# Kernel tuning notes

Hardware: AMD Instinct MI355X
Metric: run time of the kernel (lower is better)

Reference implementation:

```python
import jax, jax.numpy as jnp
import numpy as np

EPS = 1e-12
NEG = -1e30
TOPK = 20

def l2norm(x, axis):
    n = jnp.sqrt(jnp.sum(x * x, axis=axis, keepdims=True))
    return x / jnp.maximum(n, EPS)

def setup_inputs() -> dict:
    key = jax.random.key(0)
    ks = jax.random.split(key, 12)
    B, R, W, D = 128, 36, 60, 1024
    img_regions = jax.random.normal(ks[0], (B, R, D), dtype=jnp.float32)
    cap_words = jax.random.normal(ks[1], (B, W, D), dtype=jnp.float32)
    cap_len = jax.random.randint(ks[2], (B,), 10, W + 1, dtype=jnp.int32)
    s = 0.1
    return {
        "img_regions": img_regions,
        "cap_words": cap_words,
        "w1_t2i": jax.random.normal(ks[3], (TOPK, TOPK), jnp.float32) * s,
        "b1_t2i": jnp.zeros((TOPK,), jnp.float32),
        "w2_t2i": jax.random.normal(ks[4], (TOPK,), jnp.float32) * s,
        "b2_t2i": jnp.zeros((), jnp.float32),
        "w1_i2t": jax.random.normal(ks[5], (TOPK, TOPK), jnp.float32) * s,
        "b1_i2t": jnp.zeros((TOPK,), jnp.float32),
        "w2_i2t": jax.random.normal(ks[6], (TOPK,), jnp.float32) * s,
        "b2_i2t": jnp.zeros((), jnp.float32),
        "cap_len": cap_len,
    }

def _mlp(x, w1, b1, w2, b2):
    h = jax.nn.relu(x @ w1 + b1)
    return h @ w2 + b2  # Linear(topk,1).squeeze(-1)

def reference(img_regions, cap_words, w1_t2i, b1_t2i, w2_t2i, b2_t2i,
              w1_i2t, b1_i2t, w2_i2t, b2_i2t, cap_len):
    C, W, D = cap_words.shape
    I, R, _ = img_regions.shape
    img_n = l2norm(img_regions, -1)            # [I,R,D]
    cap_n = l2norm(cap_words, -1)              # [C,W,D]
    # all caption x image pair similarities: sim[c,i,w,r]
    sim = jnp.einsum('cwd,ird->ciwr', cap_n, img_n)
    sim = jnp.where(sim >= 0, sim, 0.1 * sim)  # leaky_relu(0.1) (scan=True)
    num_sel = jnp.maximum(cap_len, TOPK)       # num_selected_word per caption
    w_idx = jnp.arange(W)
    sel_mask = (w_idx[None, :] < num_sel[:, None])  # [C,W]
    cap_mask = (w_idx[None, :] < cap_len[:, None])  # [C,W]
    sel4 = sel_mask[:, None, :, None]

    # ---- t2i (row) path: normalize over word axis among selected words ----
    sim_w = sim * sel4
    norm_w = jnp.sqrt(jnp.sum(sim_w * sim_w, axis=2, keepdims=True))
    sim_w = sim_w / jnp.maximum(norm_w, EPS)
    row_sim = jnp.max(sim_w, axis=3)                      # [C,I,W]
    row_sim = jnp.where(sel_mask[:, None, :], row_sim, NEG)
    row_mean = jnp.sum(jnp.where(cap_mask[:, None, :], row_sim, 0.0), axis=2) \
               / cap_len[:, None].astype(jnp.float32)     # [C,I]
    row_topk = jax.lax.top_k(row_sim, TOPK)[0]            # [C,I,K]

    # ---- i2t (column) path: normalize over region axis, max over real words ----
    norm_r = jnp.sqrt(jnp.sum(sim * sim, axis=3, keepdims=True))
    sim_r = sim / jnp.maximum(norm_r, EPS)
    col_sim = jnp.max(jnp.where(cap_mask[:, None, :, None], sim_r, NEG), axis=2)  # [C,I,R]
    col_mean = jnp.mean(col_sim, axis=2)                  # [C,I]
    col_topk = jax.lax.top_k(col_sim, TOPK)[0]            # [C,I,K]

    batch_t2i = row_topk                                   # [C,I,K]
    batch_t2i_mean = row_mean                              # [C,I]
    batch_i2t = jnp.transpose(col_topk, (1, 0, 2))         # [I,C,K]
    batch_i2t_mean = jnp.transpose(col_mean, (1, 0))       # [I,C]

    t2i_rel = _mlp(batch_t2i, w1_t2i, b1_t2i, w2_t2i, b2_t2i) + batch_t2i_mean
    i2t_rel = _mlp(batch_i2t, w1_i2t, b1_i2t, w2_i2t, b2_i2t) + batch_i2t_mean
    return (t2i_rel, i2t_rel, batch_t2i_mean, batch_i2t_mean)
```

## Files before the change

### kernel.cpp

```cpp
#include <hip/hip_runtime.h>
#include <hip/hip_bf16.h>
#include <cstdint>
#include <cstddef>

#define C_ 128
#define I_ 128
#define W_ 60
#define R_ 36
#define D_ 1024
#define TOPK 20
#define NEGV (-1e30f)
#define EPSV (1e-12f)

typedef __attribute__((ext_vector_type(8))) short bf16x8;
typedef __attribute__((ext_vector_type(4))) float f32x4;
typedef __attribute__((ext_vector_type(4))) int i32x4;

__device__ inline float bf2f(unsigned short u) {
    union { unsigned int i; float f; } x;
    x.i = ((unsigned int)u) << 16;
    return x.f;
}
__device__ inline unsigned short f2bf(float f) {
    __hip_bfloat16 h = __float2bfloat16(f);
    return *(unsigned short*)&h;
}
__device__ inline float wave_sum(float v) {
    #pragma unroll
    for (int o = 32; o; o >>= 1) v += __shfl_xor(v, o);
    return v;
}
__device__ inline float wave_max(float v) {
    #pragma unroll
    for (int o = 32; o; o >>= 1) v = fmaxf(v, __shfl_xor(v, o));
    return v;
}
__device__ inline float loadw(const void* p, int idx, bool isF32) {
    if (isF32) return ((const float*)p)[idx];
    return bf2f(((const unsigned short*)p)[idx]);
}
__device__ inline void dma16(const void* g, void* l) {
    __builtin_amdgcn_global_load_lds(
        (const __attribute__((address_space(1))) unsigned int*)g,
        (__attribute__((address_space(3))) unsigned int*)l, 16, 0, 0);
}

__device__ inline float bitonic64_desc(float v, int lane) {
    #pragma unroll
    for (int k = 2; k <= 64; k <<= 1) {
        #pragma unroll
        for (int j = k >> 1; j > 0; j >>= 1) {
            float o = __shfl_xor(v, j);
            bool keepMax = (((lane & k) == 0) == ((lane & j) == 0));
            v = keepMax ? fmaxf(v, o) : fminf(v, o);
        }
    }
    return v;
}

__device__ inline float topk_mlp2(float val, int lane,
                                  const float* __restrict__ w1g,
                                  const float* __restrict__ b1g,
                                  const float* __restrict__ w2g, float b2v) {
    float s = bitonic64_desc(val, lane);
    float h = 0.f;
    if (lane < TOPK) h = b1g[lane];
    #pragma unroll
    for (int k = 0; k < TOPK; ++k) {
        float sk = __shfl(s, k);
        if (lane < TOPK) h += sk * w1g[k * TOPK + lane];
    }
    float contrib = 0.f;
    if (lane < TOPK) contrib = fmaxf(h, 0.f) * w2g[lane];
    contrib = wave_sum(contrib);
    return contrib + b2v;
}

__global__ __launch_bounds__(256) void prep_norm3(
    const void* __restrict__ img, const void* __restrict__ cap,
    const void* __restrict__ w1_t2i, const void* __restrict__ b1_t2i,
    const void* __restrict__ w2_t2i, const void* __restrict__ b2_t2i,
    const void* __restrict__ w1_i2t, const void* __restrict__ b1_i2t,
    const void* __restrict__ w2_i2t, const void* __restrict__ b2_i2t,
    unsigned short* __restrict__ outN, float* __restrict__ wsW) {
    int t = threadIdx.x;
    int lane = t & 63;
    int wv = t >> 6;
    unsigned int probe = ((const unsigned int*)img)[lane];
    float pa = fmaxf(__builtin_fabsf(bf2f(probe & 0xffff)),
                     __builtin_fabsf(bf2f(probe >> 16)));
    bool isF32 = __ballot(pa > 1e6f) != 0ULL;

    int row = blockIdx.x * 4 + wv;
    const void* src; int srow;
    if (row < I_ * R_) { src = img; srow = row; }
    else               { src = cap; srow = row - I_ * R_; }

    float v[16];
    if (isF32) {
        const float* p = (const float*)src + (size_t)srow * D_;
        #pragma unroll
        for (int q = 0; q < 4; ++q) {
            float4 r = *(const float4*)(p + 4 * (lane + 64 * q));
            v[4 * q] = r.x; v[4 * q + 1] = r.y; v[4 * q + 2] = r.z; v[4 * q + 3] = r.w;
        }
    } else {
        const unsigned short* p = (const unsigned short*)src + (size_t)srow * D_;
        #pragma unroll
        for (int q = 0; q < 2; ++q) {
            uint4 r = *(const uint4*)(p + 8 * (lane + 64 * q));
            v[8 * q + 0] = bf2f(r.x & 0xffff); v[8 * q + 1] = bf2f(r.x >> 16);
            v[8 * q + 2] = bf2f(r.y & 0xffff); v[8 * q + 3] = bf2f(r.y >> 16);
            v[8 * q + 4] = bf2f(r.z & 0xffff); v[8 * q + 5] = bf2f(r.z >> 16);
            v[8 * q + 6] = bf2f(r.w & 0xffff); v[8 * q + 7] = bf2f(r.w >> 16);
        }
    }
    float ss = 0.f;
    #pragma unroll
    for (int q = 0; q < 16; ++q) ss += v[q] * v[q];
    ss = wave_sum(ss);
    float s = 1.0f / fmaxf(sqrtf(ss), EPSV);
    unsigned short* dst = outN + (size_t)row * D_;
    if (isF32) {
        #pragma unroll
        for (int q = 0; q < 4; ++q) {
            uint2 w;
            w.x = (unsigned)f2bf(v[4 * q] * s)     | ((unsigned)f2bf(v[4 * q + 1] * s) << 16);
            w.y = (unsigned)f2bf(v[4 * q + 2] * s) | ((unsigned)f2bf(v[4 * q + 3] * s) << 16);
            *(uint2*)(dst + 4 * (lane + 64 * q)) = w;
        }
    } else {
        #pragma unroll
        for (int q = 0; q < 2; ++q) {
            uint4 w;
            w.x = (unsigned)f2bf(v[8 * q + 0] * s) | ((unsigned)f2bf(v[8 * q + 1] * s) << 16);
            w.y = (unsigned)f2bf(v[8 * q + 2] * s) | ((unsigned)f2bf(v[8 * q + 3] * s) << 16);
            w.z = (unsigned)f2bf(v[8 * q + 4] * s) | ((unsigned)f2bf(v[8 * q + 5] * s) << 16);
            w.w = (unsigned)f2bf(v[8 * q + 6] * s) | ((unsigned)f2bf(v[8 * q + 7] * s) << 16);
            *(uint4*)(dst + 8 * (lane + 64 * q)) = w;
        }
    }
    if (blockIdx.x == 0) {
        for (int idx = t; idx < 400; idx += 256) {
            wsW[idx]       = loadw(w1_t2i, idx, isF32);
            wsW[400 + idx] = loadw(w1_i2t, idx, isF32);
        }
        if (t < 20) {
            wsW[800 + t] = loadw(b1_t2i, t, isF32);
            wsW[820 + t] = loadw(b1_i2t, t, isF32);
            wsW[840 + t] = loadw(w2_t2i, t, isF32);
            wsW[860 + t] = loadw(w2_i2t, t, isF32);
        }
        if (t == 0) { wsW[880] = loadw(b2_t2i, 0, isF32); wsW[881] = loadw(b2_i2t, 0, isF32); }
    }
}

#define SSB 148

struct __align__(16) Smem4 {
    union {
        struct { short A[128 * 64]; short B[144 * 64]; } st;
        unsigned short Sb[120 * SSB];
    } u;
    float nw[8][36];
    float nr[8][60];
};

__global__ __launch_bounds__(256, 4) void adj_main4(
    const unsigned short* __restrict__ capN, const unsigned short* __restrict__ imgN,
    const float* __restrict__ wsW, const int* __restrict__ cap_len,
    float* __restrict__ out) {
    __shared__ Smem4 sm;
    int tid = threadIdx.x;
    int lane = tid & 63;
    int wid = tid >> 6;
    int bx = blockIdx.x;
    int cg = bx & 63;
    int ig = bx >> 6;
    int c0 = cg * 2;
    int i0 = ig * 4;

    float b2a = wsW[880], b2b = wsW[881];

    f32x4 acc0[9], acc1[9];
    #pragma unroll
    for (int t = 0; t < 9; ++t) {
        acc0[t] = (f32x4){0.f, 0.f, 0.f, 0.f};
        acc1[t] = (f32x4){0.f, 0.f, 0.f, 0.f};
    }

    const unsigned short* capB = capN + (size_t)c0 * 60 * D_;
    const unsigned short* imgB = imgN + (size_t)i0 * 36 * D_;

    int quad = lane >> 4;
    int l16 = lane & 15;
    int sub = lane >> 3;
    int q8 = (lane & 7) ^ sub;

    for (int kc = 0; kc < 16; ++kc) {
        int kb = kc * 64;
        #pragma unroll
        for (int u = 0; u < 4; ++u) {
            int wo = (wid << 2) + u;
            int r = (wo << 3) + sub;
            int ar = r < 120 ? r : 119;
            dma16(capB + (size_t)ar * D_ + kb + q8 * 8,
                  (char*)sm.u.st.A + (wo << 10));
        }
        for (int wo = wid; wo < 18; wo += 4) {
            int r = (wo << 3) + sub;
            dma16(imgB + (size_t)r * D_ + kb + q8 * 8,
                  (char*)sm.u.st.B + (wo << 10));
        }
        __syncthreads();
        #pragma unroll
        for (int ks = 0; ks < 2; ++ks) {
            int swz = ((quad + 4 * ks) ^ (l16 & 7)) << 3;
            int rowA0 = (wid << 4) + l16;
            int rowA1 = ((wid + 4) << 4) + l16;
            bf16x8 a0 = *(const bf16x8*)(sm.u.st.A + rowA0 * 64 + swz);
            bf16x8 a1 = *(const bf16x8*)(sm.u.st.A + rowA1 * 64 + swz);
            #pragma unroll
            for (int t = 0; t < 9; ++t) {
                int rowB = (t << 4) + l16;
                bf16x8 b = *(const bf16x8*)(sm.u.st.B + rowB * 64 + swz);
                acc0[t] = __builtin_amdgcn_mfma_f32_16x16x32_bf16(a0, b, acc0[t], 0, 0, 0);
                acc1[t] = __builtin_amdgcn_mfma_f32_16x16x32_bf16(a1, b, acc1[t], 0, 0, 0);
            }
        }
        __syncthreads();
    }
    #pragma unroll
    for (int t = 0; t < 9; ++t) {
        int col = 16 * t + l16;
        #pragma unroll
        for (int v = 0; v < 4; ++v) {
            int row0 = wid * 16 + quad * 4 + v;
            float x0 = acc0[t][v];
            x0 = x0 >= 0.f ? x0 : 0.1f * x0;
            sm.u.Sb[row0 * SSB + col] = f2bf(x0);
            int row1 = 64 + wid * 16 + quad * 4 + v;
            if (row1 < 120) {
                float x1 = acc1[t][v];
                x1 = x1 >= 0.f ? x1 : 0.1f * x1;
                sm.u.Sb[row1 * SSB + col] = f2bf(x1);
            }
        }
    }
    __syncthreads();

    #pragma unroll 1
    for (int pp = 0; pp < 2; ++pp) {
        int p = wid + pp * 4;
        int cc = p >> 2, j = p & 3;
        int c = c0 + cc, i = i0 + j;
        int sbase = cc * 60;
        int cbase = j * 36;
        int L = cap_len[c];
        if (L < 1) L = 1;
        if (L > 60) L = 60;
        int Msel = L > TOPK ? L : TOPK;

        if (lane < 36) {
            float ssum = 0.f;
            for (int w = 0; w < Msel; ++w) {
                float v = bf2f(sm.u.Sb[(sbase + w) * SSB + cbase + lane]);
                ssum += v * v;
            }
            sm.nw[p][lane] = 1.0f / fmaxf(sqrtf(ssum), EPSV);
        }
        if (lane < 60) {
            float ssum = 0.f;
            for (int r = 0; r < 36; ++r) {
                float v = bf2f(sm.u.Sb[(sbase + lane) * SSB + cbase + r]);
                ssum += v * v;
            }
            sm.nr[p][lane] = 1.0f / fmaxf(sqrtf(ssum), EPSV);
        }

        float rs = NEGV;
        if (lane < Msel) {
            float m = -3.4e38f;
            for (int r = 0; r < 36; ++r) {
                float v = bf2f(sm.u.Sb[(sbase + lane) * SSB + cbase + r]);
                m = fmaxf(m, v * sm.nw[p][r]);
            }
            rs = m;
        }
        float msum = (lane < L) ? rs : 0.f;
        msum = wave_sum(msum);
        float row_mean = msum / (float)L;

        float t2i = topk_mlp2(rs, lane, wsW, wsW + 800, wsW + 840, b2a) + row_mean;
        if (lane == 0) {
            out[(size_t)c * 128 + i] = t2i;
            out[2 * 16384 + (size_t)c * 128 + i] = row_mean;
        }

        float cs = NEGV;
        if (lane < 36) {
            float m = -3.4e38f;
            for (int w = 0; w < L; ++w) {
                float v = bf2f(sm.u.Sb[(sbase + w) * SSB + cbase + lane]);
                m = fmaxf(m, v * sm.nr[p][w]);
            }
            cs = m;
        }
        float csum = (lane < 36) ? cs : 0.f;
        csum = wave_sum(csum);
        float col_mean = csum / 36.f;

        float i2t = topk_mlp2(cs, lane, wsW + 400, wsW + 820, wsW + 860, b2b) + col_mean;
        if (lane == 0) {
            out[16384 + (size_t)i * 128 + c] = i2t;
            out[3 * 16384 + (size_t)i * 128 + c] = col_mean;
        }
    }
}

__device__ inline float topk_mlp(float val, int lane,
                                 const float* __restrict__ w1,
                                 const float* __restrict__ b1,
                                 const float* __restrict__ w2, float b2v) {
    float tk[TOPK];
    #pragma unroll 1
    for (int k = 0; k < TOPK; ++k) {
        float m = wave_max(val);
        tk[k] = m;
        unsigned long long msk = __ballot(val == m);
        int first = __ffsll(msk) - 1;
        if (first >= 0 && lane == first) val = NEGV;
    }
    float contrib = 0.f;
    if (lane < TOPK) {
        float h = b1[lane];
        #pragma unroll 1
        for (int k = 0; k < TOPK; ++k)
            h += tk[k] * w1[k * TOPK + lane];
        h = fmaxf(h, 0.f);
        contrib = h * w2[lane];
    }
    contrib = wave_sum(contrib);
    return contrib + b2v;
}

__global__ void detect_dtype(const unsigned short* __restrict__ probe,
                             int* __restrict__ flag) {
    if (threadIdx.x == 0) {
        float mx = 0.f;
        for (int k = 0; k < 256; ++k) {
            float v = __builtin_fabsf(bf2f(probe[k]));
            if (v > mx) mx = v;
        }
        *flag = (mx > 1e6f) ? 1 : 0;
    }
}

__global__ __launch_bounds__(256) void rownorm_scale(
    const void* __restrict__ in, float* __restrict__ sc,
    const int* __restrict__ flag) {
    int row = blockIdx.x;
    int t = threadIdx.x;
    bool isF32 = (*flag != 0);
    float v0, v1, v2, v3;
    if (isF32) {
        const float* p = (const float*)in + (size_t)row * D_;
        float4 r = *(const float4*)(p + t * 4);
        v0 = r.x; v1 = r.y; v2 = r.z; v3 = r.w;
    } else {
        const unsigned short* p = (const unsigned short*)in + (size_t)row * D_;
        uint2 raw = *(const uint2*)(p + t * 4);
        v0 = bf2f(raw.x & 0xffff); v1 = bf2f(raw.x >> 16);
        v2 = bf2f(raw.y & 0xffff); v3 = bf2f(raw.y >> 16);
    }
    float ss = v0 * v0 + v1 * v1 + v2 * v2 + v3 * v3;
    ss = wave_sum(ss);
    __shared__ float part[4];
    if ((t & 63) == 0) part[t >> 6] = ss;
    __syncthreads();
    if (t == 0) {
        float tot = part[0] + part[1] + part[2] + part[3];
        sc[row] = 1.0f / fmaxf(sqrtf(tot), EPSV);
    }
}

#define LDA 72
#define SS 145
struct __align__(16) Smem {
    union {
        struct { short A[64 * LDA]; short B[144 * LDA]; } st;
        float S[60 * SS];
    } u;
    float scw[60];
    float sci[144];
    float nw[4][36];
    float nr[4][64];
    float w1a[400], w1b[400];
    float b1a[20], b1b[20];
    float w2a[20], w2b[20];
    float b2a, b2b;
};

__global__ __launch_bounds__(256) void adj_main(
    const void* __restrict__ capRaw, const void* __restrict__ imgRaw,
    const float* __restrict__ scCap, const float* __restrict__ scImg,
    const void* __restrict__ w1_t2i, const void* __restrict__ b1_t2i,
    const void* __restrict__ w2_t2i, const void* __restrict__ b2_t2i,
    const void* __restrict__ w1_i2t, const void* __restrict__ b1_i2t,
    const void* __restrict__ w2_i2t, const void* __restrict__ b2_i2t,
    const int* __restrict__ cap_len, const int* __restrict__ flag,
    float* __restrict__ out) {
    __shared__ Smem sm;
    int tid = threadIdx.x;
    int lane = tid & 63;
    int wid = tid >> 6;
    int bx = blockIdx.x;
    int c = bx >> 5;
    int g = bx & 31;
    int i0 = g * 4;
    bool isF32 = (*flag != 0);

    if (tid < 144) ((int*)(sm.u.st.A + 60 * LDA))[tid] = 0;
    if (tid < 60) sm.scw[tid] = scCap[c * 60 + tid];
    if (tid < 144) sm.sci[tid] = scImg[i0 * 36 + tid];
    for (int idx = tid; idx < 400; idx += 256) {
        sm.w1a[idx] = loadw(w1_t2i, idx, isF32);
        sm.w1b[idx] = loadw(w1_i2t, idx, isF32);
    }
    if (tid < 20) {
        sm.b1a[tid] = loadw(b1_t2i, tid, isF32);
        sm.b1b[tid] = loadw(b1_i2t, tid, isF32);
        sm.w2a[tid] = loadw(w2_t2i, tid, isF32);
        sm.w2b[tid] = loadw(w2_i2t, tid, isF32);
    }
    if (tid == 0) { sm.b2a = loadw(b2_t2i, 0, isF32); sm.b2b = loadw(b2_i2t, 0, isF32); }

    f32x4 acc[9];
    #pragma unroll
    for (int t = 0; t < 9; ++t) acc[t] = (f32x4){0.f, 0.f, 0.f, 0.f};

    int quad = lane >> 4;
    int l16 = lane & 15;
    int aoff = (16 * wid + l16) * LDA + quad * 8;
    int boff = l16 * LDA + quad * 8;

    for (int kc = 0; kc < 16; ++kc) {
        __syncthreads();
        int kbase = kc * 64;
        if (isF32) {
            const float* capB = (const float*)capRaw + (size_t)c * W_ * D_;
            const float* imgB = (const float*)imgRaw + (size_t)i0 * R_ * D_;
            for (int idx = tid; idx < 480; idx += 256) {
                int row = idx >> 3, ch = idx & 7;
                const float* p = capB + row * D_ + kbase + ch * 8;
                float4 x = *(const float4*)p;
                float4 y = *(const float4*)(p + 4);
                unsigned int d0 = (unsigned)f2bf(x.x) | ((unsigned)f2bf(x.y) << 16);
                unsigned int d1 = (unsigned)f2bf(x.z) | ((unsigned)f2bf(x.w) << 16);
                unsigned int d2 = (unsigned)f2bf(y.x) | ((unsigned)f2bf(y.y) << 16);
                unsigned int d3 = (unsigned)f2bf(y.z) | ((unsigned)f2bf(y.w) << 16);
                *(i32x4*)(sm.u.st.A + row * LDA + ch * 8) =
                    (i32x4){(int)d0, (int)d1, (int)d2, (int)d3};
            }
            for (int idx = tid; idx < 1152; idx += 256) {
                int row = idx >> 3, ch = idx & 7;
                const float* p = imgB + row * D_ + kbase + ch * 8;
                float4 x = *(const float4*)p;
                float4 y = *(const float4*)(p + 4);
                unsigned int d0 = (unsigned)f2bf(x.x) | ((unsigned)f2bf(x.y) << 16);
                unsigned int d1 = (unsigned)f2bf(x.z) | ((unsigned)f2bf(x.w) << 16);
                unsigned int d2 = (unsigned)f2bf(y.x) | ((unsigned)f2bf(y.y) << 16);
                unsigned int d3 = (unsigned)f2bf(y.z) | ((unsigned)f2bf(y.w) << 16);
                *(i32x4*)(sm.u.st.B + row * LDA + ch * 8) =
                    (i32x4){(int)d0, (int)d1, (int)d2, (int)d3};
            }
        } else {
            const short* capB = (const short*)capRaw + (size_t)c * W_ * D_;
            const short* imgB = (const short*)imgRaw + (size_t)i0 * R_ * D_;
            for (int idx = tid; idx < 480; idx += 256) {
                int row = idx >> 3, ch = idx & 7;
                i32x4 v = *(const i32x4*)(capB + row * D_ + kbase + ch * 8);
                *(i32x4*)(sm.u.st.A + row * LDA + ch * 8) = v;
            }
            for (int idx = tid; idx < 1152; idx += 256) {
                int row = idx >> 3, ch = idx & 7;
                i32x4 v = *(const i32x4*)(imgB + row * D_ + kbase + ch * 8);
                *(i32x4*)(sm.u.st.B + row * LDA + ch * 8) = v;
            }
        }
        __syncthreads();
        #pragma unroll
        for (int ks = 0; ks < 2; ++ks) {
            bf16x8 a = *(const bf16x8*)(sm.u.st.A + aoff + 32 * ks);
            #pragma unroll
            for (int t = 0; t < 9; ++t) {
                bf16x8 b = *(const bf16x8*)(sm.u.st.B + t * (16 * LDA) + boff + 32 * ks);
                acc[t] = __builtin_amdgcn_mfma_f32_16x16x32_bf16(a, b, acc[t], 0, 0, 0);
            }
        }
    }
    __syncthreads();
    #pragma unroll
    for (int t = 0; t < 9; ++t) {
        #pragma unroll
        for (int v = 0; v < 4; ++v) {
            int row = 16 * wid + quad * 4 + v;
            int col = 16 * t + l16;
            if (row < 60) {
                float x = acc[t][v] * sm.scw[row] * sm.sci[col];
                x = x >= 0.f ? x : 0.1f * x;
                sm.u.S[row * SS + col] = x;
            }
        }
    }
    __syncthreads();

    int j = wid;
    int i = i0 + j;
    int base = 36 * j;
    int L = cap_len[c];
    if (L < 1) L = 1;
    if (L > 60) L = 60;
    int Msel = L > TOPK ? L : TOPK;

    if (lane < 36) {
        float ssum = 0.f;
        for (int w = 0; w < Msel; ++w) {
            float v = sm.u.S[w * SS + base + lane];
            ssum += v * v;
        }
        sm.nw[j][lane] = 1.0f / fmaxf(sqrtf(ssum), EPSV);
    }
    if (lane < 60) {
        float ssum = 0.f;
        for (int r = 0; r < 36; ++r) {
            float v = sm.u.S[lane * SS + base + r];
            ssum += v * v;
        }
        sm.nr[j][lane] = 1.0f / fmaxf(sqrtf(ssum), EPSV);
    }

    float rs = NEGV;
    if (lane < Msel) {
        float m = -3.4e38f;
        for (int r = 0; r < 36; ++r) {
            float v = sm.u.S[lane * SS + base + r];
            m = fmaxf(m, v * sm.nw[j][r]);
        }
        rs = m;
    }
    float msum = (lane < L) ? rs : 0.f;
    msum = wave_sum(msum);
    float row_mean = msum / (float)L;

    float t2i = topk_mlp(rs, lane, sm.w1a, sm.b1a, sm.w2a, sm.b2a) + row_mean;
    if (lane == 0) {
        out[(size_t)c * 128 + i] = t2i;
        out[2 * 16384 + (size_t)c * 128 + i] = row_mean;
    }

    float cs = NEGV;
    if (lane < 36) {
        float m = -3.4e38f;
        for (int w = 0; w < L; ++w) {
            float v = sm.u.S[w * SS + base + lane];
            m = fmaxf(m, v * sm.nr[j][w]);
        }
        cs = m;
    }
    float csum = (lane < 36) ? cs : 0.f;
    csum = wave_sum(csum);
    float col_mean = csum / 36.f;

    float i2t = topk_mlp(cs, lane, sm.w1b, sm.b1b, sm.w2b, sm.b2b) + col_mean;
    if (lane == 0) {
        out[16384 + (size_t)i * 128 + c] = i2t;
        out[3 * 16384 + (size_t)i * 128 + c] = col_mean;
    }
}

extern "C" void kernel_launch(void* const* d_in, const int* in_sizes, int n_in,
                              void* d_out, int out_size, void* d_ws, size_t ws_size,
                              hipStream_t stream) {
    (void)in_sizes; (void)n_in; (void)out_size;
    const void* img    = d_in[0];
    const void* cap    = d_in[1];
    const int* cap_len = (const int*)d_in[10];
    float* out = (float*)d_out;

    const size_t needed = 4096 + (size_t)(I_ * R_ + C_ * W_) * D_ * 2;

    if (ws_size >= needed) {
        float* wsW = (float*)d_ws;
        unsigned short* outN = (unsigned short*)((char*)d_ws + 4096);
        const unsigned short* imgN = outN;
        const unsigned short* capN = outN + (size_t)I_ * R_ * D_;
        prep_norm3<<<(I_ * R_ + C_ * W_) / 4, 256, 0, stream>>>(
            img, cap,
            d_in[2], d_in[3], d_in[4], d_in[5],
            d_in[6], d_in[7], d_in[8], d_in[9],
            outN, wsW);
        adj_main4<<<2048, 256, 0, stream>>>(capN, imgN, wsW, cap_len, out);
    } else {
        int* flag = (int*)d_ws;
        float* scImg = (float*)d_ws + 16;
        float* scCap = scImg + I_ * R_;
        detect_dtype<<<1, 64, 0, stream>>>((const unsigned short*)img, flag);
        rownorm_scale<<<I_ * R_, 256, 0, stream>>>(img, scImg, flag);
        rownorm_scale<<<C_ * W_, 256, 0, stream>>>(cap, scCap, flag);
        adj_main<<<C_ * 32, 256, 0, stream>>>(cap, img, scCap, scImg,
                                              d_in[2], d_in[3], d_in[4], d_in[5],
                                              d_in[6], d_in[7], d_in[8], d_in[9],
                                              cap_len, flag, out);
    }
}
```

Measured before the change: 219.7 us.

## Double-buffer GEMM K-loop with async LDS prefetch and vectorize epilogue reads

The bf16 MFMA main loop moves from 16 single-buffered 64-wide K chunks to 32 double-buffered 32-wide chunks. Each chunk's global-to-LDS DMA is issued before computing on the previous buffer, and the loop needs one barrier per iteration instead of two. The load addressing is precomputed once with a new XOR swizzle. The row-norm and row-max epilogue loops now read LDS as uint2 words, four bf16 values at a time. The cost is more address registers and smaller K steps, which may affect occupancy at 4 blocks per SM.

```diff
diff --git a/kernel.cpp b/kernel.cpp
--- a/kernel.cpp
+++ b/kernel.cpp
@@ -157,20 +157,20 @@
 
 #define SSB 148
 
-struct __align__(16) Smem4 {
+struct __align__(16) Smem5 {
     union {
-        struct { short A[128 * 64]; short B[144 * 64]; } st;
+        struct { short A[2][128 * 32]; short B[2][144 * 32]; } st;
         unsigned short Sb[120 * SSB];
     } u;
     float nw[8][36];
     float nr[8][60];
 };
 
-__global__ __launch_bounds__(256, 4) void adj_main4(
+__global__ __launch_bounds__(256, 4) void adj_main5(
     const unsigned short* __restrict__ capN, const unsigned short* __restrict__ imgN,
     const float* __restrict__ wsW, const int* __restrict__ cap_len,
     float* __restrict__ out) {
-    __shared__ Smem4 sm;
+    __shared__ Smem5 sm;
     int tid = threadIdx.x;
     int lane = tid & 63;
     int wid = tid >> 6;
@@ -194,42 +194,69 @@
 
     int quad = lane >> 4;
     int l16 = lane & 15;
-    int sub = lane >> 3;
-    int q8 = (lane & 7) ^ sub;
-
-    for (int kc = 0; kc < 16; ++kc) {
-        int kb = kc * 64;
-        #pragma unroll
-        for (int u = 0; u < 4; ++u) {
-            int wo = (wid << 2) + u;
-            int r = (wo << 3) + sub;
+    int rloc = lane >> 2;
+    int pch = lane & 3;
+
+    const char* gp[5];
+    unsigned lo[5][2];
+    bool val[5];
+    #pragma unroll
+    for (int s = 0; s < 5; ++s) {
+        int wo = wid + 4 * s;
+        val[s] = wo < 17;
+        int woc = val[s] ? wo : 0;
+        if (woc < 8) {
+            int r = woc * 16 + rloc;
             int ar = r < 120 ? r : 119;
-            dma16(capB + (size_t)ar * D_ + kb + q8 * 8,
-                  (char*)sm.u.st.A + (wo << 10));
-        }
-        for (int wo = wid; wo < 18; wo += 4) {
-            int r = (wo << 3) + sub;
-            dma16(imgB + (size_t)r * D_ + kb + q8 * 8,
-                  (char*)sm.u.st.B + (wo << 10));
-        }
+            gp[s] = (const char*)(capB + (size_t)ar * D_) +
+                    ((pch ^ ((r >> 1) & 3)) << 4);
+            lo[s][0] = (unsigned)(woc << 10);
+            lo[s][1] = (unsigned)(8192 + (woc << 10));
+        } else {
+            int r = (woc - 8) * 16 + rloc;
+            gp[s] = (const char*)(imgB + (size_t)r * D_) +
+                    ((pch ^ ((r >> 1) & 3)) << 4);
+            lo[s][0] = (unsigned)(16384 + ((woc - 8) << 10));
+            lo[s][1] = (unsigned)(16384 + 9216 + ((woc - 8) << 10));
+        }
+    }
+    int arow0 = wid * 16 + l16;
+    int arow1 = arow0 + 64;
+    int aswz = (quad ^ ((arow0 >> 1) & 3)) << 3;
+    int aofs0 = arow0 * 32 + aswz;
+    int aofs1 = arow1 * 32 + aswz;
+    int bofs[9];
+    #pragma unroll
+    for (int t = 0; t < 9; ++t) {
+        int br = t * 16 + l16;
+        bofs[t] = br * 32 + ((quad ^ ((br >> 1) & 3)) << 3);
+    }
+
+    #pragma unroll
+    for (int s = 0; s < 5; ++s)
+        if (val[s]) dma16(gp[s], (char*)&sm + lo[s][0]);
+
+    for (int kc = 0; kc < 32; ++kc) {
+        int d = kc & 1;
         __syncthreads();
-        #pragma unroll
-        for (int ks = 0; ks < 2; ++ks) {
-            int swz = ((quad + 4 * ks) ^ (l16 & 7)) << 3;
-            int rowA0 = (wid << 4) + l16;
-            int rowA1 = ((wid + 4) << 4) + l16;
-            bf16x8 a0 = *(const bf16x8*)(sm.u.st.A + rowA0 * 64 + swz);
-            bf16x8 a1 = *(const bf16x8*)(sm.u.st.A + rowA1 * 64 + swz);
+        if (kc + 1 < 32) {
+            int gofs = (kc + 1) << 6;
             #pragma unroll
-            for (int t = 0; t < 9; ++t) {
-                int rowB = (t << 4) + l16;
-                bf16x8 b = *(const bf16x8*)(sm.u.st.B + rowB * 64 + swz);
-                acc0[t] = __builtin_amdgcn_mfma_f32_16x16x32_bf16(a0, b, acc0[t], 0, 0, 0);
-                acc1[t] = __builtin_amdgcn_mfma_f32_16x16x32_bf16(a1, b, acc1[t], 0, 0, 0);
-            }
-        }
-        __syncthreads();
-    }
+            for (int s = 0; s < 5; ++s)
+                if (val[s]) dma16(gp[s] + gofs, (char*)&sm + lo[s][d ^ 1]);
+        }
+        const short* aP = sm.u.st.A[d];
+        const short* bP = sm.u.st.B[d];
+        bf16x8 a0 = *(const bf16x8*)(aP + aofs0);
+        bf16x8 a1 = *(const bf16x8*)(aP + aofs1);
+        #pragma unroll
+        for (int t = 0; t < 9; ++t) {
+            bf16x8 b = *(const bf16x8*)(bP + bofs[t]);
+            acc0[t] = __builtin_amdgcn_mfma_f32_16x16x32_bf16(a0, b, acc0[t], 0, 0, 0);
+            acc1[t] = __builtin_amdgcn_mfma_f32_16x16x32_bf16(a1, b, acc1[t], 0, 0, 0);
+        }
+    }
+    __syncthreads();
     #pragma unroll
     for (int t = 0; t < 9; ++t) {
         int col = 16 * t + l16;
@@ -270,20 +297,29 @@
             sm.nw[p][lane] = 1.0f / fmaxf(sqrtf(ssum), EPSV);
         }
         if (lane < 60) {
+            const uint2* rp = (const uint2*)(sm.u.Sb + (sbase + lane) * SSB + cbase);
             float ssum = 0.f;
-            for (int r = 0; r < 36; ++r) {
-                float v = bf2f(sm.u.Sb[(sbase + lane) * SSB + cbase + r]);
-                ssum += v * v;
+            #pragma unroll
+            for (int q = 0; q < 9; ++q) {
+                uint2 u = rp[q];
+                float a = bf2f(u.x & 0xffff), b = bf2f(u.x >> 16);
+                float e = bf2f(u.y & 0xffff), f = bf2f(u.y >> 16);
+                ssum += a * a + b * b + e * e + f * f;
             }
             sm.nr[p][lane] = 1.0f / fmaxf(sqrtf(ssum), EPSV);
         }
 
         float rs = NEGV;
         if (lane < Msel) {
+            const uint2* rp = (const uint2*)(sm.u.Sb + (sbase + lane) * SSB + cbase);
             float m = -3.4e38f;
-            for (int r = 0; r < 36; ++r) {
-                float v = bf2f(sm.u.Sb[(sbase + lane) * SSB + cbase + r]);
-                m = fmaxf(m, v * sm.nw[p][r]);
+            #pragma unroll
+            for (int q = 0; q < 9; ++q) {
+                uint2 u = rp[q];
+                m = fmaxf(m, bf2f(u.x & 0xffff) * sm.nw[p][4 * q]);
+                m = fmaxf(m, bf2f(u.x >> 16)    * sm.nw[p][4 * q + 1]);
+                m = fmaxf(m, bf2f(u.y & 0xffff) * sm.nw[p][4 * q + 2]);
+                m = fmaxf(m, bf2f(u.y >> 16)    * sm.nw[p][4 * q + 3]);
             }
             rs = m;
         }
@@ -600,7 +636,7 @@
             d_in[2], d_in[3], d_in[4], d_in[5],
             d_in[6], d_in[7], d_in[8], d_in[9],
             outN, wsW);
-        adj_main4<<<2048, 256, 0, stream>>>(capN, imgN, wsW, cap_len, out);
+        adj_main5<<<2048, 256, 0, stream>>>(capN, imgN, wsW, cap_len, out);
     } else {
         int* flag = (int*)d_ws;
         float* scImg = (float*)d_ws + 16;
```

Result: slower. 230.0 us (+4.7%).

## Compute column norms and column max from MFMA accumulators in registers

Applied to the files above, without the earlier changes.

Moves the word-axis squared-sum (for t2i normalization) and the masked word-max (for i2t) into the accumulator epilogue, reducing across lanes with shuffles and packing partial results into a small shared array. Row norms and row max now read shared memory as vectorized uint2 loads with unrolled loops instead of scalar strided loops. This removes serial per-lane loops over up to 60 words that read strided shared memory. In exchange it adds extra barriers, more shared memory, bf16 rounding of the partial sums and maxima, and a second pass over the accumulators.

```diff
diff --git a/kernel.cpp b/kernel.cpp
--- a/kernel.cpp
+++ b/kernel.cpp
@@ -157,20 +157,21 @@
 
 #define SSB 148
 
-struct __align__(16) Smem4 {
+struct __align__(16) Smem6 {
     union {
         struct { short A[128 * 64]; short B[144 * 64]; } st;
         unsigned short Sb[120 * SSB];
     } u;
     float nw[8][36];
     float nr[8][60];
+    unsigned int pw[4][144];
 };
 
-__global__ __launch_bounds__(256, 4) void adj_main4(
+__global__ __launch_bounds__(256, 4) void adj_main6(
     const unsigned short* __restrict__ capN, const unsigned short* __restrict__ imgN,
     const float* __restrict__ wsW, const int* __restrict__ cap_len,
     float* __restrict__ out) {
-    __shared__ Smem4 sm;
+    __shared__ Smem6 sm;
     int tid = threadIdx.x;
     int lane = tid & 63;
     int wid = tid >> 6;
@@ -181,6 +182,10 @@
     int i0 = ig * 4;
 
     float b2a = wsW[880], b2b = wsW[881];
+    int L0 = cap_len[c0];     if (L0 < 1) L0 = 1; if (L0 > 60) L0 = 60;
+    int L1 = cap_len[c0 + 1]; if (L1 < 1) L1 = 1; if (L1 > 60) L1 = 60;
+    int M0 = L0 > TOPK ? L0 : TOPK;
+    int M1 = L1 > TOPK ? L1 : TOPK;
 
     f32x4 acc0[9], acc1[9];
     #pragma unroll
@@ -230,60 +235,118 @@
         }
         __syncthreads();
     }
+
     #pragma unroll
     for (int t = 0; t < 9; ++t) {
         int col = 16 * t + l16;
+        float sA = 0.f, sB = 0.f;
         #pragma unroll
         for (int v = 0; v < 4; ++v) {
             int row0 = wid * 16 + quad * 4 + v;
             float x0 = acc0[t][v];
             x0 = x0 >= 0.f ? x0 : 0.1f * x0;
             sm.u.Sb[row0 * SSB + col] = f2bf(x0);
-            int row1 = 64 + wid * 16 + quad * 4 + v;
+            bool c1 = row0 >= 60;
+            int w0 = c1 ? row0 - 60 : row0;
+            float x2 = x0 * x0;
+            if (!c1 && w0 < M0) sA += x2;
+            if ( c1 && w0 < M1) sB += x2;
+            int row1 = row0 + 64;
             if (row1 < 120) {
                 float x1 = acc1[t][v];
                 x1 = x1 >= 0.f ? x1 : 0.1f * x1;
                 sm.u.Sb[row1 * SSB + col] = f2bf(x1);
-            }
-        }
+                int w1 = row1 - 60;
+                if (w1 < M1) sB += x1 * x1;
+            }
+        }
+        sA += __shfl_xor(sA, 16); sA += __shfl_xor(sA, 32);
+        sB += __shfl_xor(sB, 16); sB += __shfl_xor(sB, 32);
+        if (quad == 0)
+            sm.pw[wid][col] = ((unsigned)f2bf(sA) << 16) | (unsigned)f2bf(sB);
     }
     __syncthreads();
 
     #pragma unroll 1
     for (int pp = 0; pp < 2; ++pp) {
-        int p = wid + pp * 4;
-        int cc = p >> 2, j = p & 3;
+        int p = wid + 4 * pp;
+        int sbase = pp * 60;
+        int cbase = wid * 36;
+        if (lane < 60) {
+            const uint2* rp = (const uint2*)(sm.u.Sb + (sbase + lane) * SSB + cbase);
+            float ssum = 0.f;
+            #pragma unroll
+            for (int q = 0; q < 9; ++q) {
+                uint2 u = rp[q];
+                float a = bf2f(u.x & 0xffff), b = bf2f(u.x >> 16);
+                float e = bf2f(u.y & 0xffff), f = bf2f(u.y >> 16);
+                ssum += a * a + b * b + e * e + f * f;
+            }
+            sm.nr[p][lane] = 1.0f / fmaxf(sqrtf(ssum), EPSV);
+        }
+        if (lane < 36) {
+            float s = 0.f;
+            #pragma unroll
+            for (int wv = 0; wv < 4; ++wv) {
+                unsigned u = sm.pw[wv][cbase + lane];
+                s += bf2f(pp ? (unsigned short)(u & 0xffff)
+                             : (unsigned short)(u >> 16));
+            }
+            sm.nw[p][lane] = 1.0f / fmaxf(sqrtf(s), EPSV);
+        }
+    }
+    __syncthreads();
+
+    #pragma unroll
+    for (int t = 0; t < 9; ++t) {
+        int col = 16 * t + l16;
+        int jt = col / 36;
+        float mA = NEGV, mB = NEGV;
+        #pragma unroll
+        for (int v = 0; v < 4; ++v) {
+            int row0 = wid * 16 + quad * 4 + v;
+            float x0 = acc0[t][v];
+            x0 = x0 >= 0.f ? x0 : 0.1f * x0;
+            bool c1 = row0 >= 60;
+            int w0 = c1 ? row0 - 60 : row0;
+            if (!c1) { if (w0 < L0) mA = fmaxf(mA, x0 * sm.nr[jt][w0]); }
+            else     { if (w0 < L1) mB = fmaxf(mB, x0 * sm.nr[4 + jt][w0]); }
+            int row1 = row0 + 64;
+            if (row1 < 120) {
+                float x1 = acc1[t][v];
+                x1 = x1 >= 0.f ? x1 : 0.1f * x1;
+                int w1 = row1 - 60;
+                if (w1 < L1) mB = fmaxf(mB, x1 * sm.nr[4 + jt][w1]);
+            }
+        }
+        mA = fmaxf(mA, __shfl_xor(mA, 16)); mA = fmaxf(mA, __shfl_xor(mA, 32));
+        mB = fmaxf(mB, __shfl_xor(mB, 16)); mB = fmaxf(mB, __shfl_xor(mB, 32));
+        if (quad == 0)
+            sm.pw[wid][col] = ((unsigned)f2bf(mA) << 16) | (unsigned)f2bf(mB);
+    }
+    __syncthreads();
+
+    #pragma unroll 1
+    for (int pp = 0; pp < 2; ++pp) {
+        int p = wid + 4 * pp;
+        int cc = pp, j = wid;
         int c = c0 + cc, i = i0 + j;
         int sbase = cc * 60;
         int cbase = j * 36;
-        int L = cap_len[c];
-        if (L < 1) L = 1;
-        if (L > 60) L = 60;
-        int Msel = L > TOPK ? L : TOPK;
-
-        if (lane < 36) {
-            float ssum = 0.f;
-            for (int w = 0; w < Msel; ++w) {
-                float v = bf2f(sm.u.Sb[(sbase + w) * SSB + cbase + lane]);
-                ssum += v * v;
-            }
-            sm.nw[p][lane] = 1.0f / fmaxf(sqrtf(ssum), EPSV);
-        }
-        if (lane < 60) {
-            float ssum = 0.f;
-            for (int r = 0; r < 36; ++r) {
-                float v = bf2f(sm.u.Sb[(sbase + lane) * SSB + cbase + r]);
-                ssum += v * v;
-            }
-            sm.nr[p][lane] = 1.0f / fmaxf(sqrtf(ssum), EPSV);
-        }
+        int L = cc ? L1 : L0;
+        int Msel = cc ? M1 : M0;
 
         float rs = NEGV;
         if (lane < Msel) {
+            const uint2* rp = (const uint2*)(sm.u.Sb + (sbase + lane) * SSB + cbase);
             float m = -3.4e38f;
-            for (int r = 0; r < 36; ++r) {
-                float v = bf2f(sm.u.Sb[(sbase + lane) * SSB + cbase + r]);
-                m = fmaxf(m, v * sm.nw[p][r]);
+            #pragma unroll
+            for (int q = 0; q < 9; ++q) {
+                uint2 u = rp[q];
+                m = fmaxf(m, bf2f(u.x & 0xffff) * sm.nw[p][4 * q]);
+                m = fmaxf(m, bf2f(u.x >> 16)    * sm.nw[p][4 * q + 1]);
+                m = fmaxf(m, bf2f(u.y & 0xffff) * sm.nw[p][4 * q + 2]);
+                m = fmaxf(m, bf2f(u.y >> 16)    * sm.nw[p][4 * q + 3]);
             }
             rs = m;
         }
@@ -299,10 +362,12 @@
 
         float cs = NEGV;
         if (lane < 36) {
-            float m = -3.4e38f;
-            for (int w = 0; w < L; ++w) {
-                float v = bf2f(sm.u.Sb[(sbase + w) * SSB + cbase + lane]);
-                m = fmaxf(m, v * sm.nr[p][w]);
+            float m = NEGV;
+            #pragma unroll
+            for (int wv = 0; wv < 4; ++wv) {
+                unsigned u = sm.pw[wv][cbase + lane];
+                m = fmaxf(m, bf2f(cc ? (unsigned short)(u & 0xffff)
+                                     : (unsigned short)(u >> 16)));
             }
             cs = m;
         }
@@ -600,7 +665,7 @@
             d_in[2], d_in[3], d_in[4], d_in[5],
             d_in[6], d_in[7], d_in[8], d_in[9],
             outN, wsW);
-        adj_main4<<<2048, 256, 0, stream>>>(capN, imgN, wsW, cap_len, out);
+        adj_main6<<<2048, 256, 0, stream>>>(capN, imgN, wsW, cap_len, out);
     } else {
         int* flag = (int*)d_ws;
         float* scImg = (float*)d_ws + 16;
```

Result: slower. 226.0 us (+2.9%).
